# Performance work log

Measured on AMD Instinct MI355X. Metric: run time of the kernel, lower is better.

The kernel has to match this reference:

```python
import jax, jax.numpy as jnp
import numpy as np
import math

B, T, EMB, HD = 4, 2048, 2048, 128
HALF = HD // 2


def setup_inputs() -> dict:
    key = jax.random.key(0)
    ks = jax.random.split(key, 4)
    x = jax.random.normal(ks[0], (B, T, EMB), dtype=jnp.float32)
    s = 1.0 / math.sqrt(EMB)
    Wq = jax.random.normal(ks[1], (EMB, HD), dtype=jnp.float32) * s
    Wk = jax.random.normal(ks[2], (EMB, HD), dtype=jnp.float32) * s
    Wv = jax.random.normal(ks[3], (EMB, HD), dtype=jnp.float32) * s
    # Standard RoPE rotation table: theta_i = 10000^(-2i/HD), angle = pos * theta
    inv_freq = 1.0 / (10000.0 ** (np.arange(0, HALF, dtype=np.float32) / HALF))
    angles = np.arange(T, dtype=np.float32)[:, None] * inv_freq[None, :]  # [T, HALF]
    rot_cos = jnp.asarray(np.cos(angles), dtype=jnp.float32)
    rot_sin = jnp.asarray(np.sin(angles), dtype=jnp.float32)
    # Additive causal mask: 0 on/below diagonal, -1e9 above
    NEG = -1e9
    mask = jnp.where(jnp.tril(jnp.ones((T, T), dtype=bool)), 0.0, NEG).astype(jnp.float32)
    return {"x": x, "Wq": Wq, "Wk": Wk, "Wv": Wv,
            "rot_cos": rot_cos, "rot_sin": rot_sin, "mask": mask}


def _apply_rope(q, rot_cos, rot_sin):
    # q: [B, T, HD]; view last dim as HALF complex pairs and rotate
    qp = q.reshape(q.shape[0], q.shape[1], HALF, 2)
    re, im = qp[..., 0], qp[..., 1]
    out_re = re * rot_cos - im * rot_sin  # broadcast [T,HALF] over batch
    out_im = re * rot_sin + im * rot_cos
    return jnp.stack([out_re, out_im], axis=-1).reshape(q.shape)


def reference(x, Wq, Wk, Wv, rot_cos, rot_sin, mask):
    Q = x @ Wq  # [B, T, HD]
    K = x @ Wk
    V = x @ Wv
    Q = _apply_rope(Q, rot_cos, rot_sin)
    K = _apply_rope(K, rot_cos, rot_sin)
    scores = jnp.einsum('bqd,bkd->bqk', Q, K) / math.sqrt(HD)
    probs = jax.nn.softmax(scores + mask, axis=-1)  # dropout is identity in eval
    return jnp.einsum('bqk,bkd->bqd', probs, V)
```

## Files before the change

kernel.cpp:

```cpp
#include <hip/hip_runtime.h>
#include <cstddef>
#include <cstdint>

#define T_SEQ 2048
#define EMB_D 2048
#define HD_D  128

typedef __attribute__((ext_vector_type(8))) short short8;
typedef __attribute__((ext_vector_type(4))) float f32x4;
typedef __attribute__((ext_vector_type(4))) unsigned short ushort4v;
typedef __attribute__((ext_vector_type(8))) unsigned short ushort8v;

union frag_u { short8 s8; unsigned u[4]; };

static __device__ __forceinline__ unsigned short f2bf_rne(float f) {
    union { float f; unsigned u; } v; v.f = f;
    unsigned r = v.u + 0x7fffu + ((v.u >> 16) & 1u);
    return (unsigned short)(r >> 16);
}
static __device__ __forceinline__ unsigned short f2bf_fast(float f) {
    union { float f; unsigned u; } v; v.f = f;
    return (unsigned short)((v.u + 0x8000u) >> 16);
}
static __device__ __forceinline__ unsigned pk2(float a, float b) {
    union { float f; unsigned u; } x, y; x.f = a; y.f = b;
    return __builtin_amdgcn_perm(y.u + 0x8000u, x.u + 0x8000u, 0x07060302);
}
static __device__ __forceinline__ void dma16(const void* g, void* l) {
    __builtin_amdgcn_global_load_lds(
        (const __attribute__((address_space(1))) unsigned int*)g,
        (__attribute__((address_space(3))) unsigned int*)l, 16, 0, 0);
}
#define EXP2F(x) __builtin_amdgcn_exp2f(x)

__global__ __launch_bounds__(256) void prep_weights(
    const float* __restrict__ Wq, const float* __restrict__ Wk,
    const float* __restrict__ Wv, unsigned short* __restrict__ Wt)
{
    __shared__ __attribute__((aligned(16))) unsigned short tw[64 * 132];
    const int w = blockIdx.y;
    const int k0 = blockIdx.x * 64;
    const float* W = (w == 0) ? Wq : (w == 1) ? Wk : Wv;
    const int tid = threadIdx.x;
#pragma unroll
    for (int p = 0; p < 8; p++) {
        const int f = p * 256 + tid;
        const int row = f >> 5, c4 = f & 31;
        const float4 v = *(const float4*)&W[(size_t)(k0 + row) * HD_D + c4 * 4];
        ushort4v h = { f2bf_rne(v.x), f2bf_rne(v.y), f2bf_rne(v.z), f2bf_rne(v.w) };
        *(ushort4v*)&tw[row * 132 + c4 * 4] = h;
    }
    __syncthreads();
    const int n = tid >> 1, h = tid & 1;
    unsigned short* dst = Wt + (size_t)w * (HD_D * EMB_D) + (size_t)n * EMB_D + k0 + h * 32;
#pragma unroll
    for (int j = 0; j < 4; j++) {
        ushort8v o;
#pragma unroll
        for (int jj = 0; jj < 8; jj++) o[jj] = tw[(h * 32 + j * 8 + jj) * 132 + n];
        *(ushort8v*)&dst[j * 8] = o;
    }
}

__global__ __launch_bounds__(256, 1) void qkv_fused(
    const float* __restrict__ x, const unsigned short* __restrict__ Wt,
    const float* __restrict__ rcos, const float* __restrict__ rsin,
    unsigned short* __restrict__ Qb, unsigned short* __restrict__ Kb,
    unsigned short* __restrict__ Vt)
{
    __shared__ __attribute__((aligned(16))) float xs[32 * 64];
    __shared__ __attribute__((aligned(16))) unsigned short wsb[384 * 64];
    const int m0 = blockIdx.x * 32;
    const int tid = threadIdx.x;
    const int lane = tid & 63, wave = tid >> 6;
    const int l15 = lane & 15, lq = lane >> 4;

    const float* xSrc[2]; float* xDst[2];
#pragma unroll
    for (int p = 0; p < 2; p++) {
        const int g = p * 256 + tid;
        const int row = g >> 4, c = g & 15;
        xSrc[p] = x + (size_t)(m0 + row) * EMB_D + (c ^ (row & 15)) * 4;
        xDst[p] = xs + (size_t)(p * 256 + wave * 64) * 4;
    }
    const unsigned short* wSrc[12]; unsigned short* wDst[12];
#pragma unroll
    for (int p = 0; p < 12; p++) {
        const int g = p * 256 + tid;
        const int n = g >> 3, c = g & 7;
        wSrc[p] = Wt + (size_t)n * EMB_D + (c ^ (n & 7)) * 8;
        wDst[p] = wsb + (size_t)(p * 256 + wave * 64) * 8;
    }

    int offA[2][2][2];
#pragma unroll
    for (int i = 0; i < 2; i++)
#pragma unroll
        for (int ks = 0; ks < 2; ks++) {
            const int row = i * 16 + l15;
            const int ga = ks * 8 + lq * 2;
            offA[i][ks][0] = row * 64 + ((ga)     ^ (row & 15)) * 4;
            offA[i][ks][1] = row * 64 + ((ga + 1) ^ (row & 15)) * 4;
        }
    int offB[6][2];
#pragma unroll
    for (int j = 0; j < 6; j++)
#pragma unroll
        for (int ks = 0; ks < 2; ks++) {
            const int n = wave * 96 + j * 16 + l15;
            const int gb = ks * 4 + lq;
            offB[j][ks] = n * 64 + (gb ^ (n & 7)) * 8;
        }

    f32x4 acc[2][6];
#pragma unroll
    for (int i = 0; i < 2; i++)
#pragma unroll
        for (int j = 0; j < 6; j++) acc[i][j] = (f32x4){0.f, 0.f, 0.f, 0.f};

    for (int k0 = 0; k0 < EMB_D; k0 += 64) {
        __syncthreads();
#pragma unroll
        for (int p = 0; p < 2; p++)  dma16(xSrc[p] + k0, xDst[p]);
#pragma unroll
        for (int p = 0; p < 12; p++) dma16(wSrc[p] + k0, wDst[p]);
        __syncthreads();

        frag_u A[2][2];
#pragma unroll
        for (int i = 0; i < 2; i++)
#pragma unroll
            for (int ks = 0; ks < 2; ks++) {
                const f32x4 f0 = *(const f32x4*)&xs[offA[i][ks][0]];
                const f32x4 f1 = *(const f32x4*)&xs[offA[i][ks][1]];
                A[i][ks].u[0] = pk2(f0.x, f0.y);
                A[i][ks].u[1] = pk2(f0.z, f0.w);
                A[i][ks].u[2] = pk2(f1.x, f1.y);
                A[i][ks].u[3] = pk2(f1.z, f1.w);
            }
#pragma unroll
        for (int ks = 0; ks < 2; ks++)
#pragma unroll
            for (int j = 0; j < 6; j++) {
                const short8 B = *(const short8*)&wsb[offB[j][ks]];
#pragma unroll
                for (int i = 0; i < 2; i++)
                    acc[i][j] = __builtin_amdgcn_mfma_f32_16x16x32_bf16(
                        A[i][ks].s8, B, acc[i][j], 0, 0, 0);
            }
    }

    const float qscale = 0.08838834764831845f * 1.4426950408889634f;
#pragma unroll
    for (int i = 0; i < 2; i++) {
#pragma unroll
        for (int r = 0; r < 4; r++) {
            const int row = m0 + i * 16 + lq * 4 + r;
            const int t = row & (T_SEQ - 1);
            const int bb = row >> 11;
#pragma unroll
            for (int j = 0; j < 6; j++) {
                const int col = wave * 96 + j * 16 + l15;
                const int mat = col >> 7, mcol = col & 127;
                const float v = acc[i][j][r];
                if (mat == 2) {
                    Vt[((size_t)bb * HD_D + mcol) * T_SEQ + t] = f2bf_rne(v);
                } else {
                    const int ip = mcol >> 1;
                    const float c = rcos[t * 64 + ip];
                    const float s = rsin[t * 64 + ip];
                    const float pv = __shfl_xor(v, 1);
                    float rv = (mcol & 1) ? (pv * s + v * c) : (v * c - pv * s);
                    if (mat == 0) {
                        rv *= qscale;
                        Qb[(size_t)row * HD_D + mcol] = f2bf_rne(rv);
                    } else {
                        Kb[(size_t)row * HD_D + mcol] = f2bf_rne(rv);
                    }
                }
            }
        }
    }
}

__global__ __launch_bounds__(256, 2) void attn(
    const unsigned short* __restrict__ Qb, const unsigned short* __restrict__ Kb,
    const unsigned short* __restrict__ Vt, float* __restrict__ out)
{
    __shared__ float O_s[4][16 * 128];
    __shared__ __attribute__((aligned(16))) unsigned short P_s[4][2][16 * 40];
    __shared__ float l_s[4][16];

    const int tid = threadIdx.x;
    const int lane = tid & 63, wave = tid >> 6;
    const int l15 = lane & 15, lq = lane >> 4;
    const int kf = lq * 8;

    const int b  = blockIdx.x & 3;
    const int q0 = (127 - (blockIdx.x >> 2)) * 16;
    const int kend = q0 + 16;
    const float M2 = 16.0f;

    const unsigned short* Qp = Qb + (size_t)(b * T_SEQ + q0) * HD_D;
    short8 aQ[4];
#pragma unroll
    for (int d = 0; d < 4; d++)
        aQ[d] = *(const short8*)&Qp[l15 * HD_D + d * 32 + kf];

    f32x4 acc[8];
#pragma unroll
    for (int d = 0; d < 8; d++) acc[d] = (f32x4){0.f, 0.f, 0.f, 0.f};
    float l_r[4] = {0.f, 0.f, 0.f, 0.f};

    const unsigned short* Kbase = Kb + (size_t)b * T_SEQ * HD_D;
    const unsigned short* Vbase = Vt + (size_t)b * HD_D * T_SEQ;
    unsigned short* PwA = &P_s[wave][0][0];
    unsigned short* PwB = &P_s[wave][1][0];

    for (int c = wave; c * 32 < kend; c += 8) {
        const int kA = c * 32;
        const int kB = (c + 4) * 32;
        const bool hB = kB < kend;

        const unsigned short* KpA = Kbase + (size_t)kA * HD_D;
        const unsigned short* KpB = Kbase + (size_t)kB * HD_D;
        short8 KA[8], KB_[8];
#pragma unroll
        for (int d = 0; d < 4; d++)
#pragma unroll
            for (int n = 0; n < 2; n++)
                KA[d * 2 + n] = *(const short8*)&KpA[(size_t)(n * 16 + l15) * HD_D + d * 32 + kf];
        if (hB) {
#pragma unroll
            for (int d = 0; d < 4; d++)
#pragma unroll
                for (int n = 0; n < 2; n++)
                    KB_[d * 2 + n] = *(const short8*)&KpB[(size_t)(n * 16 + l15) * HD_D + d * 32 + kf];
        }

        f32x4 sA0 = (f32x4){0.f, 0.f, 0.f, 0.f}, sA1 = sA0, sB0 = sA0, sB1 = sA0;
#pragma unroll
        for (int d = 0; d < 4; d++) {
            sA0 = __builtin_amdgcn_mfma_f32_16x16x32_bf16(aQ[d], KA[d * 2 + 0], sA0, 0, 0, 0);
            sA1 = __builtin_amdgcn_mfma_f32_16x16x32_bf16(aQ[d], KA[d * 2 + 1], sA1, 0, 0, 0);
        }
        if (hB) {
#pragma unroll
            for (int d = 0; d < 4; d++) {
                sB0 = __builtin_amdgcn_mfma_f32_16x16x32_bf16(aQ[d], KB_[d * 2 + 0], sB0, 0, 0, 0);
                sB1 = __builtin_amdgcn_mfma_f32_16x16x32_bf16(aQ[d], KB_[d * 2 + 1], sB1, 0, 0, 0);
            }
        }

        short8 VA[8];
#pragma unroll
        for (int d = 0; d < 8; d++)
            VA[d] = *(const short8*)&Vbase[(size_t)(d * 16 + l15) * T_SEQ + kA + kf];

#pragma unroll
        for (int r = 0; r < 4; r++) {
            const int q = q0 + lq * 4 + r;
            const float p0 = ((kA + l15)      <= q) ? EXP2F(sA0[r] - M2) : 0.f;
            const float p1 = ((kA + 16 + l15) <= q) ? EXP2F(sA1[r] - M2) : 0.f;
            l_r[r] += p0 + p1;
            const int prow = (lq * 4 + r) * 40;
            PwA[prow + l15]      = f2bf_fast(p0);
            PwA[prow + 16 + l15] = f2bf_fast(p1);
        }
        const short8 pA = *(const short8*)&PwA[l15 * 40 + kf];
#pragma unroll
        for (int d = 0; d < 8; d++)
            acc[d] = __builtin_amdgcn_mfma_f32_16x16x32_bf16(pA, VA[d], acc[d], 0, 0, 0);

        if (hB) {
            short8 VB[8];
#pragma unroll
            for (int d = 0; d < 8; d++)
                VB[d] = *(const short8*)&Vbase[(size_t)(d * 16 + l15) * T_SEQ + kB + kf];
#pragma unroll
            for (int r = 0; r < 4; r++) {
                const int q = q0 + lq * 4 + r;
                const float p0 = ((kB + l15)      <= q) ? EXP2F(sB0[r] - M2) : 0.f;
                const float p1 = ((kB + 16 + l15) <= q) ? EXP2F(sB1[r] - M2) : 0.f;
                l_r[r] += p0 + p1;
                const int prow = (lq * 4 + r) * 40;
                PwB[prow + l15]      = f2bf_fast(p0);
                PwB[prow + 16 + l15] = f2bf_fast(p1);
            }
            const short8 pB = *(const short8*)&PwB[l15 * 40 + kf];
#pragma unroll
            for (int d = 0; d < 8; d++)
                acc[d] = __builtin_amdgcn_mfma_f32_16x16x32_bf16(pB, VB[d], acc[d], 0, 0, 0);
        }
    }

#pragma unroll
    for (int r = 0; r < 4; r++) {
        float lr = l_r[r];
        lr += __shfl_xor(lr, 1);
        lr += __shfl_xor(lr, 2);
        lr += __shfl_xor(lr, 4);
        lr += __shfl_xor(lr, 8);
        if (l15 == 0) l_s[wave][lq * 4 + r] = lr;
#pragma unroll
        for (int d = 0; d < 8; d++)
            O_s[wave][(lq * 4 + r) * 128 + d * 16 + l15] = acc[d][r];
    }
    __syncthreads();

    const int row = tid >> 4;
    const int dc = (tid & 15) * 8;
    const float lt = l_s[0][row] + l_s[1][row] + l_s[2][row] + l_s[3][row];
    const float inv = 1.0f / lt;
    f32x4 o0 = (f32x4){0.f, 0.f, 0.f, 0.f};
    f32x4 o1 = (f32x4){0.f, 0.f, 0.f, 0.f};
#pragma unroll
    for (int w2 = 0; w2 < 4; w2++) {
        const float* p = &O_s[w2][row * 128 + dc];
        o0 += *(const f32x4*)p;
        o1 += *(const f32x4*)(p + 4);
    }
    float* op = out + (size_t)(b * T_SEQ + q0 + row) * HD_D + dc;
    *(f32x4*)op       = o0 * inv;
    *(f32x4*)(op + 4) = o1 * inv;
}

extern "C" void kernel_launch(void* const* d_in, const int* in_sizes, int n_in,
                              void* d_out, int out_size, void* d_ws, size_t ws_size,
                              hipStream_t stream)
{
    (void)in_sizes; (void)n_in; (void)out_size; (void)ws_size;
    const float* x  = (const float*)d_in[0];
    const float* Wq = (const float*)d_in[1];
    const float* Wk = (const float*)d_in[2];
    const float* Wv = (const float*)d_in[3];
    const float* rc = (const float*)d_in[4];
    const float* rs = (const float*)d_in[5];
    float* out = (float*)d_out;

    char* ws = (char*)d_ws;
    unsigned short* Wt = (unsigned short*)(ws);
    unsigned short* Qb = (unsigned short*)(ws + 1572864);
    unsigned short* Kb = (unsigned short*)(ws + 1572864 + 2097152);
    unsigned short* Vt = (unsigned short*)(ws + 1572864 + 2 * 2097152);

    prep_weights<<<dim3(32, 3), 256, 0, stream>>>(Wq, Wk, Wv, Wt);
    qkv_fused   <<<dim3(256),   256, 0, stream>>>(x, Wt, rc, rs, Qb, Kb, Vt);
    attn        <<<dim3(512),   256, 0, stream>>>(Qb, Kb, Vt, out);
}
```

Measured before the change: 203.5 us.

## Split QKV projection over column halves, load weights directly into registers, double-buffer x

The QKV projection kernel now launches twice as many blocks, each computing half of the 384 output columns. Weight fragments are read straight from global memory into registers instead of being staged through shared memory. The x tile is double-buffered in shared memory so the next tile's async copy overlaps the current MFMA work. This cuts shared-memory traffic and LDS size and raises occupancy, but it reads x twice overall and relies on cache hits for the uncoalesced-pattern weight loads.

Measured after the change: 219.4 us. 7.8% more time.

```diff
diff --git a/kernel.cpp b/kernel.cpp
--- a/kernel.cpp
+++ b/kernel.cpp
@@ -62,34 +62,37 @@
     }
 }
 
-__global__ __launch_bounds__(256, 1) void qkv_fused(
+__global__ __launch_bounds__(256, 2) void qkv_fused(
     const float* __restrict__ x, const unsigned short* __restrict__ Wt,
     const float* __restrict__ rcos, const float* __restrict__ rsin,
     unsigned short* __restrict__ Qb, unsigned short* __restrict__ Kb,
     unsigned short* __restrict__ Vt)
 {
-    __shared__ __attribute__((aligned(16))) float xs[32 * 64];
-    __shared__ __attribute__((aligned(16))) unsigned short wsb[384 * 64];
-    const int m0 = blockIdx.x * 32;
+    __shared__ __attribute__((aligned(16))) float xs[2][32 * 64];
+    const int nh = blockIdx.x & 1;
+    const int m0 = (blockIdx.x >> 1) * 32;
     const int tid = threadIdx.x;
     const int lane = tid & 63, wave = tid >> 6;
     const int l15 = lane & 15, lq = lane >> 4;
-
-    const float* xSrc[2]; float* xDst[2];
+    const int kf = lq * 8;
+
+    const float* xSrc[2];
+    int xOff[2];
 #pragma unroll
     for (int p = 0; p < 2; p++) {
         const int g = p * 256 + tid;
         const int row = g >> 4, c = g & 15;
         xSrc[p] = x + (size_t)(m0 + row) * EMB_D + (c ^ (row & 15)) * 4;
-        xDst[p] = xs + (size_t)(p * 256 + wave * 64) * 4;
-    }
-    const unsigned short* wSrc[12]; unsigned short* wDst[12];
-#pragma unroll
-    for (int p = 0; p < 12; p++) {
-        const int g = p * 256 + tid;
-        const int n = g >> 3, c = g & 7;
-        wSrc[p] = Wt + (size_t)n * EMB_D + (c ^ (n & 7)) * 8;
-        wDst[p] = wsb + (size_t)(p * 256 + wave * 64) * 8;
+        xOff[p] = (p * 256 + wave * 64) * 4;
+    }
+
+    const unsigned short* Bp[3];
+#pragma unroll
+    for (int j = 0; j < 3; j++) {
+        const int col0 = nh * 192 + wave * 48 + j * 16;
+        const int wsel = col0 >> 7;
+        Bp[j] = Wt + (size_t)wsel * (HD_D * EMB_D)
+                   + (size_t)((col0 & 127) + l15) * EMB_D + kf;
     }
 
     int offA[2][2][2];
@@ -102,37 +105,38 @@
             offA[i][ks][0] = row * 64 + ((ga)     ^ (row & 15)) * 4;
             offA[i][ks][1] = row * 64 + ((ga + 1) ^ (row & 15)) * 4;
         }
-    int offB[6][2];
-#pragma unroll
-    for (int j = 0; j < 6; j++)
-#pragma unroll
-        for (int ks = 0; ks < 2; ks++) {
-            const int n = wave * 96 + j * 16 + l15;
-            const int gb = ks * 4 + lq;
-            offB[j][ks] = n * 64 + (gb ^ (n & 7)) * 8;
-        }
-
-    f32x4 acc[2][6];
+
+    f32x4 acc[2][3];
 #pragma unroll
     for (int i = 0; i < 2; i++)
 #pragma unroll
-        for (int j = 0; j < 6; j++) acc[i][j] = (f32x4){0.f, 0.f, 0.f, 0.f};
+        for (int j = 0; j < 3; j++) acc[i][j] = (f32x4){0.f, 0.f, 0.f, 0.f};
+
+#pragma unroll
+    for (int p = 0; p < 2; p++) dma16(xSrc[p], &xs[0][xOff[p]]);
 
     for (int k0 = 0; k0 < EMB_D; k0 += 64) {
+        const int buf = (k0 >> 6) & 1;
         __syncthreads();
-#pragma unroll
-        for (int p = 0; p < 2; p++)  dma16(xSrc[p] + k0, xDst[p]);
-#pragma unroll
-        for (int p = 0; p < 12; p++) dma16(wSrc[p] + k0, wDst[p]);
-        __syncthreads();
+        if (k0 + 64 < EMB_D) {
+#pragma unroll
+            for (int p = 0; p < 2; p++)
+                dma16(xSrc[p] + k0 + 64, &xs[buf ^ 1][xOff[p]]);
+        }
+        short8 Bf[3][2];
+#pragma unroll
+        for (int j = 0; j < 3; j++)
+#pragma unroll
+            for (int ks = 0; ks < 2; ks++)
+                Bf[j][ks] = *(const short8*)(Bp[j] + k0 + ks * 32);
 
         frag_u A[2][2];
 #pragma unroll
         for (int i = 0; i < 2; i++)
 #pragma unroll
             for (int ks = 0; ks < 2; ks++) {
-                const f32x4 f0 = *(const f32x4*)&xs[offA[i][ks][0]];
-                const f32x4 f1 = *(const f32x4*)&xs[offA[i][ks][1]];
+                const f32x4 f0 = *(const f32x4*)&xs[buf][offA[i][ks][0]];
+                const f32x4 f1 = *(const f32x4*)&xs[buf][offA[i][ks][1]];
                 A[i][ks].u[0] = pk2(f0.x, f0.y);
                 A[i][ks].u[1] = pk2(f0.z, f0.w);
                 A[i][ks].u[2] = pk2(f1.x, f1.y);
@@ -141,13 +145,11 @@
 #pragma unroll
         for (int ks = 0; ks < 2; ks++)
 #pragma unroll
-            for (int j = 0; j < 6; j++) {
-                const short8 B = *(const short8*)&wsb[offB[j][ks]];
+            for (int j = 0; j < 3; j++)
 #pragma unroll
                 for (int i = 0; i < 2; i++)
                     acc[i][j] = __builtin_amdgcn_mfma_f32_16x16x32_bf16(
-                        A[i][ks].s8, B, acc[i][j], 0, 0, 0);
-            }
+                        A[i][ks].s8, Bf[j][ks], acc[i][j], 0, 0, 0);
     }
 
     const float qscale = 0.08838834764831845f * 1.4426950408889634f;
@@ -159,8 +161,8 @@
             const int t = row & (T_SEQ - 1);
             const int bb = row >> 11;
 #pragma unroll
-            for (int j = 0; j < 6; j++) {
-                const int col = wave * 96 + j * 16 + l15;
+            for (int j = 0; j < 3; j++) {
+                const int col = nh * 192 + wave * 48 + j * 16 + l15;
                 const int mat = col >> 7, mcol = col & 127;
                 const float v = acc[i][j][r];
                 if (mat == 2) {
@@ -345,6 +347,6 @@
     unsigned short* Vt = (unsigned short*)(ws + 1572864 + 2 * 2097152);
 
     prep_weights<<<dim3(32, 3), 256, 0, stream>>>(Wq, Wk, Wv, Wt);
-    qkv_fused   <<<dim3(256),   256, 0, stream>>>(x, Wt, rc, rs, Qb, Kb, Vt);
+    qkv_fused   <<<dim3(512),   256, 0, stream>>>(x, Wt, rc, rs, Qb, Kb, Vt);
     attn        <<<dim3(512),   256, 0, stream>>>(Qb, Kb, Vt, out);
 }
```

## Double-buffer LDS tiles in QKV projection GEMM to overlap loads with MFMA

Applied to the files above, without the earlier changes.

Splits the x and weight shared-memory tiles into two buffers and issues the async global-to-LDS copy for the next K-slice before computing on the current one. This drops one barrier per iteration and is meant to hide global load latency behind the MFMA work. It doubles the LDS footprint of the projection kernel to about 112 KB, which still fits the single block per CU set by the launch bounds. Correctness relies on the barrier at the top of the loop waiting for the outstanding async copies.

Measured after the change: 205.7 us. No clear change (+1.1%).

```diff
diff --git a/kernel.cpp b/kernel.cpp
--- a/kernel.cpp
+++ b/kernel.cpp
@@ -68,28 +68,29 @@
     unsigned short* __restrict__ Qb, unsigned short* __restrict__ Kb,
     unsigned short* __restrict__ Vt)
 {
-    __shared__ __attribute__((aligned(16))) float xs[32 * 64];
-    __shared__ __attribute__((aligned(16))) unsigned short wsb[384 * 64];
+    __shared__ __attribute__((aligned(16))) float xs[2][32 * 64];
+    __shared__ __attribute__((aligned(16))) unsigned short wsb[2][384 * 64];
     const int m0 = blockIdx.x * 32;
     const int tid = threadIdx.x;
     const int lane = tid & 63, wave = tid >> 6;
     const int l15 = lane & 15, lq = lane >> 4;
-
-    const float* xSrc[2]; float* xDst[2];
+    const int kf = lq * 8;
+
+    const float* xSrc[2]; int xOff[2];
 #pragma unroll
     for (int p = 0; p < 2; p++) {
         const int g = p * 256 + tid;
         const int row = g >> 4, c = g & 15;
         xSrc[p] = x + (size_t)(m0 + row) * EMB_D + (c ^ (row & 15)) * 4;
-        xDst[p] = xs + (size_t)(p * 256 + wave * 64) * 4;
-    }
-    const unsigned short* wSrc[12]; unsigned short* wDst[12];
+        xOff[p] = (p * 256 + wave * 64) * 4;
+    }
+    const unsigned short* wSrc[12]; int wOff[12];
 #pragma unroll
     for (int p = 0; p < 12; p++) {
         const int g = p * 256 + tid;
         const int n = g >> 3, c = g & 7;
         wSrc[p] = Wt + (size_t)n * EMB_D + (c ^ (n & 7)) * 8;
-        wDst[p] = wsb + (size_t)(p * 256 + wave * 64) * 8;
+        wOff[p] = (p * 256 + wave * 64) * 8;
     }
 
     int offA[2][2][2];
@@ -118,21 +119,30 @@
 #pragma unroll
         for (int j = 0; j < 6; j++) acc[i][j] = (f32x4){0.f, 0.f, 0.f, 0.f};
 
+#pragma unroll
+    for (int p = 0; p < 2; p++)  dma16(xSrc[p], &xs[0][xOff[p]]);
+#pragma unroll
+    for (int p = 0; p < 12; p++) dma16(wSrc[p], &wsb[0][wOff[p]]);
+
     for (int k0 = 0; k0 < EMB_D; k0 += 64) {
+        const int buf = (k0 >> 6) & 1;
         __syncthreads();
-#pragma unroll
-        for (int p = 0; p < 2; p++)  dma16(xSrc[p] + k0, xDst[p]);
-#pragma unroll
-        for (int p = 0; p < 12; p++) dma16(wSrc[p] + k0, wDst[p]);
-        __syncthreads();
+        if (k0 + 64 < EMB_D) {
+#pragma unroll
+            for (int p = 0; p < 2; p++)
+                dma16(xSrc[p] + k0 + 64, &xs[buf ^ 1][xOff[p]]);
+#pragma unroll
+            for (int p = 0; p < 12; p++)
+                dma16(wSrc[p] + k0 + 64, &wsb[buf ^ 1][wOff[p]]);
+        }
 
         frag_u A[2][2];
 #pragma unroll
         for (int i = 0; i < 2; i++)
 #pragma unroll
             for (int ks = 0; ks < 2; ks++) {
-                const f32x4 f0 = *(const f32x4*)&xs[offA[i][ks][0]];
-                const f32x4 f1 = *(const f32x4*)&xs[offA[i][ks][1]];
+                const f32x4 f0 = *(const f32x4*)&xs[buf][offA[i][ks][0]];
+                const f32x4 f1 = *(const f32x4*)&xs[buf][offA[i][ks][1]];
                 A[i][ks].u[0] = pk2(f0.x, f0.y);
                 A[i][ks].u[1] = pk2(f0.z, f0.w);
                 A[i][ks].u[2] = pk2(f1.x, f1.y);
@@ -142,7 +152,7 @@
         for (int ks = 0; ks < 2; ks++)
 #pragma unroll
             for (int j = 0; j < 6; j++) {
-                const short8 B = *(const short8*)&wsb[offB[j][ks]];
+                const short8 B = *(const short8*)&wsb[buf][offB[j][ks]];
 #pragma unroll
                 for (int i = 0; i < 2; i++)
                     acc[i][j] = __builtin_amdgcn_mfma_f32_16x16x32_bf16(
```
